# Optimization experiments

Measured on AMD Instinct MI355X. Metric: run time of the kernel, lower is better.

Reference implementation:

```python
import jax, jax.numpy as jnp
import numpy as np

M, K, N = 8192, 4096, 4096

def setup_inputs() -> dict:
    key = jax.random.key(0)
    k1, k2, k3, k4, k5, k6 = jax.random.split(key, 6)
    # quantized activations (per-token symmetric int8)
    x_q = jax.random.randint(k1, (M, K), -128, 128, dtype=jnp.int32).astype(jnp.int8)
    # quantized weight (asymmetric per-output-channel): w_fp16 = scale_weight * (w_q + zp_weight)
    weight = jax.random.randint(k2, (N, K), -128, 128, dtype=jnp.int32).astype(jnp.int8)
    scale_input = (jax.random.uniform(k3, (M,), jnp.float32) * 0.009 + 0.001).astype(jnp.float16)
    scale_weight = (jax.random.uniform(k4, (N,), jnp.float32) * 0.009 + 0.001).astype(jnp.float16)
    zp_weight = jax.random.randint(k5, (N,), 100, 156, dtype=jnp.int32).astype(jnp.int16)
    bias = (jax.random.normal(k6, (N,), jnp.float32) * 0.01).astype(jnp.float16)
    # per-row sum of quantized activations (needed for zero-point correction)
    sum_input = jnp.sum(x_q.astype(jnp.int32), axis=-1).astype(jnp.float32)
    return {
        "input": x_q,
        "weight": weight,
        "bias": bias,
        "scale_input": scale_input,
        "scale_weight": scale_weight,
        "sum_input": sum_input,
        "zp_weight": zp_weight,
    }

def reference(input, weight, bias, scale_input, scale_weight, sum_input, zp_weight):
    acc = jnp.matmul(input.astype(jnp.int32), weight.astype(jnp.int32).T)
    # asymmetric weight zero-point correction: + zp_n * sum_k(x_q[m, k])
    corr = sum_input[:, None] * zp_weight.astype(jnp.float32)[None, :]
    # fused dequant epilogue: per-row activation scale * per-col weight scale, + bias
    scale = scale_input.astype(jnp.float32)[:, None] * scale_weight.astype(jnp.float32)[None, :]
    out = (acc.astype(jnp.float32) + corr) * scale + bias.astype(jnp.float32)[None, :]
    return out.astype(jnp.float16)
```

## Files before the change

### kernel.cpp

```cpp
#include <hip/hip_runtime.h>
#include <hip/hip_bf16.h>
#include <stdint.h>


#define BM 128
#define BN 128
#define BK 128

typedef __attribute__((ext_vector_type(4))) int int32x4;

__device__ __forceinline__ void async_copy16(const uint8_t* g, uint8_t* l) {
  __builtin_amdgcn_global_load_lds(
      (const __attribute__((address_space(1))) uint32_t*)(const void*)g,
      (__attribute__((address_space(3))) uint32_t*)l,
      16, 0, 0);
}

__global__ __launch_bounds__(256) void pack_kernel(
    const int* __restrict__ A, const int* __restrict__ B,
    uint8_t* __restrict__ A8, uint8_t* __restrict__ B8,
    int nA4, int nTot4) {
  int t = blockIdx.x * blockDim.x + threadIdx.x;
  if (t >= nTot4) return;
  const int4* src;
  uint32_t* dst;
  if (t < nA4) {
    src = (const int4*)A + t;
    dst = (uint32_t*)A8 + t;
  } else {
    int u = t - nA4;
    src = (const int4*)B + u;
    dst = (uint32_t*)B8 + u;
  }
  int4 v = *src;
  *dst = (uint32_t)(v.x & 255) | ((uint32_t)(v.y & 255) << 8) |
         ((uint32_t)(v.z & 255) << 16) | ((uint32_t)(v.w & 255) << 24);
}

__global__ __launch_bounds__(256) void w8a8_gemm(
    const uint8_t* __restrict__ A8, const uint8_t* __restrict__ B8,
    const float* __restrict__ bias,
    const float* __restrict__ s_in,
    const float* __restrict__ s_w,
    const float* __restrict__ sum_in,
    const int* __restrict__ zp_w,
    float* __restrict__ out,
    int M, int N, int K) {
  __shared__ uint8_t As[BM * BK];
  __shared__ uint8_t Bs[BN * BK];

  const int tid = threadIdx.x;
  const int bm = blockIdx.y, bn = blockIdx.x;
  const int row0 = bm * BM, col0 = bn * BN;
  const int wave = tid >> 6, lane = tid & 63;
  const int quad = lane >> 4, r = lane & 15;
  const int wm = (wave >> 1) * 64, wn = (wave & 1) * 64;
  const size_t sK = (size_t)K;

  const int row_s = tid >> 3;
  const int cg = (tid & 7) ^ ((tid >> 4) & 7);
  const int ldst = tid * 16;

  int32x4 acc[4][4] = {};

  for (int k0 = 0; k0 < K; k0 += BK) {
#pragma unroll
    for (int p = 0; p < 4; ++p) {
      const int rr = p * 32 + row_s;
      async_copy16(A8 + (size_t)(row0 + rr) * sK + k0 + cg * 16,
                   &As[p * 4096 + ldst]);
      async_copy16(B8 + (size_t)(col0 + rr) * sK + k0 + cg * 16,
                   &Bs[p * 4096 + ldst]);
    }
    __syncthreads();

#pragma unroll
    for (int s = 0; s < 2; ++s) {
      int32x4 afrag[4], bfrag[4];
      const int swzr = (r >> 1) & 7;
      const int cslot = ((s * 4 + quad) ^ swzr) * 16;
#pragma unroll
      for (int i = 0; i < 4; ++i)
        afrag[i] = *(const int32x4*)&As[(wm + i * 16 + r) * BK + cslot];
#pragma unroll
      for (int j = 0; j < 4; ++j)
        bfrag[j] = *(const int32x4*)&Bs[(wn + j * 16 + r) * BK + cslot];
#pragma unroll
      for (int i = 0; i < 4; ++i)
#pragma unroll
        for (int j = 0; j < 4; ++j)
          acc[i][j] = __builtin_amdgcn_mfma_i32_16x16x64_i8(
              afrag[i], bfrag[j], acc[i][j], 0, 0, 0);
    }
    __syncthreads();
  }

  float swj[4], zpj[4], bj[4];
#pragma unroll
  for (int j = 0; j < 4; ++j) {
    int gc = col0 + wn + j * 16 + r;
    swj[j] = s_w[gc];
    zpj[j] = (float)zp_w[gc];
    bj[j] = bias[gc];
  }
#pragma unroll
  for (int i = 0; i < 4; ++i) {
#pragma unroll
    for (int t = 0; t < 4; ++t) {
      int gr = row0 + wm + i * 16 + quad * 4 + t;
      float siv = s_in[gr];
      float suv = sum_in[gr];
      float* orow = out + (size_t)gr * N + col0 + wn + r;
#pragma unroll
      for (int j = 0; j < 4; ++j) {
        float v = ((float)acc[i][j][t] + suv * zpj[j]) * (siv * swj[j]) + bj[j];
        orow[j * 16] = v;
      }
    }
  }
}

__global__ __launch_bounds__(256) void w8a8_gemm_fallback(
    const int* __restrict__ A32, const int* __restrict__ B32,
    const float* __restrict__ bias,
    const float* __restrict__ s_in,
    const float* __restrict__ s_w,
    const float* __restrict__ sum_in,
    const int* __restrict__ zp_w,
    float* __restrict__ out,
    int M, int N, int K) {
  __shared__ uint8_t As[128 * 64];
  __shared__ uint8_t Bs[128 * 64];
  const int tid = threadIdx.x;
  const int bm = blockIdx.y, bn = blockIdx.x;
  const int row0 = bm * 128, col0 = bn * 128;
  const int wave = tid >> 6, lane = tid & 63;
  const int quad = lane >> 4, r = lane & 15;
  const int wm = (wave >> 1) * 64, wn = (wave & 1) * 64;
  const int lin = tid * 16;
  const int srow = lin >> 6;
  const int scol = lin & 63;
  const size_t sK = (size_t)K;
  int32x4 acc[4][4] = {};
  for (int k0 = 0; k0 < K; k0 += 64) {
#pragma unroll
    for (int c = 0; c < 2; ++c) {
      const int* ag = A32 + (size_t)(row0 + srow + c * 64) * sK + k0 + scol;
      const int* bg = B32 + (size_t)(col0 + srow + c * 64) * sK + k0 + scol;
      int32x4 pa, pb;
#pragma unroll
      for (int q = 0; q < 4; ++q) {
        int4 va = ((const int4*)ag)[q];
        int4 vb = ((const int4*)bg)[q];
        pa[q] = (int)((uint32_t)(va.x & 255) | ((uint32_t)(va.y & 255) << 8) |
                      ((uint32_t)(va.z & 255) << 16) | ((uint32_t)(va.w & 255) << 24));
        pb[q] = (int)((uint32_t)(vb.x & 255) | ((uint32_t)(vb.y & 255) << 8) |
                      ((uint32_t)(vb.z & 255) << 16) | ((uint32_t)(vb.w & 255) << 24));
      }
      *(int32x4*)&As[lin + c * 4096] = pa;
      *(int32x4*)&Bs[lin + c * 4096] = pb;
    }
    __syncthreads();
    int32x4 afrag[4], bfrag[4];
#pragma unroll
    for (int i = 0; i < 4; ++i)
      afrag[i] = *(const int32x4*)&As[(wm + i * 16 + r) * 64 + quad * 16];
#pragma unroll
    for (int j = 0; j < 4; ++j)
      bfrag[j] = *(const int32x4*)&Bs[(wn + j * 16 + r) * 64 + quad * 16];
#pragma unroll
    for (int i = 0; i < 4; ++i)
#pragma unroll
      for (int j = 0; j < 4; ++j)
        acc[i][j] = __builtin_amdgcn_mfma_i32_16x16x64_i8(afrag[i], bfrag[j],
                                                          acc[i][j], 0, 0, 0);
    __syncthreads();
  }
  float swj[4], zpj[4], bj[4];
#pragma unroll
  for (int j = 0; j < 4; ++j) {
    int gc = col0 + wn + j * 16 + r;
    swj[j] = s_w[gc];
    zpj[j] = (float)zp_w[gc];
    bj[j] = bias[gc];
  }
#pragma unroll
  for (int i = 0; i < 4; ++i) {
#pragma unroll
    for (int t = 0; t < 4; ++t) {
      int gr = row0 + wm + i * 16 + quad * 4 + t;
      float siv = s_in[gr];
      float suv = sum_in[gr];
      float* orow = out + (size_t)gr * N + col0 + wn + r;
#pragma unroll
      for (int j = 0; j < 4; ++j) {
        float v = ((float)acc[i][j][t] + suv * zpj[j]) * (siv * swj[j]) + bj[j];
        orow[j * 16] = v;
      }
    }
  }
}

extern "C" void kernel_launch(void* const* d_in, const int* in_sizes, int n_in,
                              void* d_out, int out_size, void* d_ws, size_t ws_size,
                              hipStream_t stream) {
  const int* x_q = (const int*)d_in[0];
  const int* w_q = (const int*)d_in[1];
  const float* bias = (const float*)d_in[2];
  const float* s_in = (const float*)d_in[3];
  const float* s_w = (const float*)d_in[4];
  const float* sum_in = (const float*)d_in[5];
  const int* zp_w = (const int*)d_in[6];
  float* out = (float*)d_out;

  const int M = in_sizes[3];
  const int N = in_sizes[2];
  const int K = in_sizes[0] / M;

  const size_t needA = (size_t)M * K;
  const size_t needB = (size_t)N * K;
  dim3 grid(N / BN, M / BM), block(256);

  if (ws_size >= needA + needB) {
    uint8_t* A8 = (uint8_t*)d_ws;
    uint8_t* B8 = A8 + needA;
    const int nA4 = (int)(needA / 4);
    const int nTot4 = (int)((needA + needB) / 4);
    pack_kernel<<<(nTot4 + 255) / 256, 256, 0, stream>>>(x_q, w_q, A8, B8,
                                                         nA4, nTot4);
    w8a8_gemm<<<grid, block, 0, stream>>>(A8, B8, bias, s_in, s_w, sum_in,
                                          zp_w, out, M, N, K);
  } else {
    w8a8_gemm_fallback<<<grid, block, 0, stream>>>(x_q, w_q, bias, s_in, s_w,
                                                   sum_in, zp_w, out, M, N, K);
  }
}
```

Before: 422.0 us.

## Switch int8 GEMM to 32x32x32 MFMA tiles with nontemporal loads and stores

Replaces the 16x16x64 int8 MFMA with the 32x32x32 variant, so each wave computes a 2x2 grid of 32x32 accumulators. This changes the LDS fragment indexing and the epilogue row mapping to match. The larger instruction shape means fewer LDS fragment reads per MFMA. The pack kernel now uses nontemporal loads, and the epilogue writes output with nontemporal stores to reduce cache pollution. The main risks are the different MFMA throughput and a changed pattern of LDS bank conflicts under the existing swizzle.

```diff
diff --git a/kernel.cpp b/kernel.cpp
--- a/kernel.cpp
+++ b/kernel.cpp
@@ -8,6 +8,7 @@
 #define BK 128
 
 typedef __attribute__((ext_vector_type(4))) int int32x4;
+typedef __attribute__((ext_vector_type(16))) int int32x16;
 
 __device__ __forceinline__ void async_copy16(const uint8_t* g, uint8_t* l) {
   __builtin_amdgcn_global_load_lds(
@@ -22,17 +23,17 @@
     int nA4, int nTot4) {
   int t = blockIdx.x * blockDim.x + threadIdx.x;
   if (t >= nTot4) return;
-  const int4* src;
+  const int32x4* src;
   uint32_t* dst;
   if (t < nA4) {
-    src = (const int4*)A + t;
+    src = (const int32x4*)A + t;
     dst = (uint32_t*)A8 + t;
   } else {
     int u = t - nA4;
-    src = (const int4*)B + u;
+    src = (const int32x4*)B + u;
     dst = (uint32_t*)B8 + u;
   }
-  int4 v = *src;
+  int32x4 v = __builtin_nontemporal_load(src);
   *dst = (uint32_t)(v.x & 255) | ((uint32_t)(v.y & 255) << 8) |
          ((uint32_t)(v.z & 255) << 16) | ((uint32_t)(v.w & 255) << 24);
 }
@@ -53,7 +54,7 @@
   const int bm = blockIdx.y, bn = blockIdx.x;
   const int row0 = bm * BM, col0 = bn * BN;
   const int wave = tid >> 6, lane = tid & 63;
-  const int quad = lane >> 4, r = lane & 15;
+  const int m32 = lane & 31, half = lane >> 5;
   const int wm = (wave >> 1) * 64, wn = (wave & 1) * 64;
   const size_t sK = (size_t)K;
 
@@ -61,7 +62,7 @@
   const int cg = (tid & 7) ^ ((tid >> 4) & 7);
   const int ldst = tid * 16;
 
-  int32x4 acc[4][4] = {};
+  int32x16 acc[2][2] = {};
 
   for (int k0 = 0; k0 < K; k0 += BK) {
 #pragma unroll
@@ -74,47 +75,47 @@
     }
     __syncthreads();
 
-#pragma unroll
-    for (int s = 0; s < 2; ++s) {
-      int32x4 afrag[4], bfrag[4];
-      const int swzr = (r >> 1) & 7;
-      const int cslot = ((s * 4 + quad) ^ swzr) * 16;
-#pragma unroll
-      for (int i = 0; i < 4; ++i)
-        afrag[i] = *(const int32x4*)&As[(wm + i * 16 + r) * BK + cslot];
-#pragma unroll
-      for (int j = 0; j < 4; ++j)
-        bfrag[j] = *(const int32x4*)&Bs[(wn + j * 16 + r) * BK + cslot];
-#pragma unroll
-      for (int i = 0; i < 4; ++i)
-#pragma unroll
-        for (int j = 0; j < 4; ++j)
-          acc[i][j] = __builtin_amdgcn_mfma_i32_16x16x64_i8(
+    const int swzr = (m32 >> 1) & 7;
+#pragma unroll
+    for (int ks = 0; ks < 4; ++ks) {
+      const int gran = ((ks * 2 + half) ^ swzr) * 16;
+      int32x4 afrag[2], bfrag[2];
+#pragma unroll
+      for (int i = 0; i < 2; ++i)
+        afrag[i] = *(const int32x4*)&As[(wm + i * 32 + m32) * BK + gran];
+#pragma unroll
+      for (int j = 0; j < 2; ++j)
+        bfrag[j] = *(const int32x4*)&Bs[(wn + j * 32 + m32) * BK + gran];
+#pragma unroll
+      for (int i = 0; i < 2; ++i)
+#pragma unroll
+        for (int j = 0; j < 2; ++j)
+          acc[i][j] = __builtin_amdgcn_mfma_i32_32x32x32_i8(
               afrag[i], bfrag[j], acc[i][j], 0, 0, 0);
     }
     __syncthreads();
   }
 
-  float swj[4], zpj[4], bj[4];
-#pragma unroll
-  for (int j = 0; j < 4; ++j) {
-    int gc = col0 + wn + j * 16 + r;
+  float swj[2], zpj[2], bj[2];
+#pragma unroll
+  for (int j = 0; j < 2; ++j) {
+    int gc = col0 + wn + j * 32 + m32;
     swj[j] = s_w[gc];
     zpj[j] = (float)zp_w[gc];
     bj[j] = bias[gc];
   }
 #pragma unroll
-  for (int i = 0; i < 4; ++i) {
-#pragma unroll
-    for (int t = 0; t < 4; ++t) {
-      int gr = row0 + wm + i * 16 + quad * 4 + t;
+  for (int i = 0; i < 2; ++i) {
+#pragma unroll
+    for (int reg = 0; reg < 16; ++reg) {
+      int gr = row0 + wm + i * 32 + (reg & 3) + 8 * (reg >> 2) + 4 * half;
       float siv = s_in[gr];
       float suv = sum_in[gr];
-      float* orow = out + (size_t)gr * N + col0 + wn + r;
-#pragma unroll
-      for (int j = 0; j < 4; ++j) {
-        float v = ((float)acc[i][j][t] + suv * zpj[j]) * (siv * swj[j]) + bj[j];
-        orow[j * 16] = v;
+      float* orow = out + (size_t)gr * N + col0 + wn + m32;
+#pragma unroll
+      for (int j = 0; j < 2; ++j) {
+        float v = ((float)acc[i][j][reg] + suv * zpj[j]) * (siv * swj[j]) + bj[j];
+        __builtin_nontemporal_store(v, &orow[j * 32]);
       }
     }
   }
```

Measured after the change: 406.3 us. 3.7% less time.
